# Kernel optimization log

Measured on AMD Instinct MI355X. Metric: run time of the kernel, lower is better.

The kernel has to match this reference:

```python
import jax, jax.numpy as jnp
import numpy as np

NUM_SCIENTISTS = 1_000_000
NUM_PAPERS = 100_000
EMB_DIM = 64
B = 262_144            # number of (scientist, paper) rating pairs
TOTAL_IMPLICIT = 5_242_880  # total flattened implicit-feedback paper ids (avg 20/row)
GLOBAL_MEAN = 3.82


def setup_inputs() -> dict:
    key = jax.random.key(0)
    ks = jax.random.split(key, 8)
    scientist_ids = jax.random.randint(ks[0], (B,), 0, NUM_SCIENTISTS, dtype=jnp.int32)
    paper_ids = jax.random.randint(ks[1], (B,), 0, NUM_PAPERS, dtype=jnp.int32)
    flat_papers = jax.random.randint(ks[2], (TOTAL_IMPLICIT,), 0, NUM_PAPERS, dtype=jnp.int32)
    # sorted segment ids: CSR-style ragged mapping implicit papers -> batch row
    segment_ids = jnp.sort(jax.random.randint(ks[3], (TOTAL_IMPLICIT,), 0, B, dtype=jnp.int32))
    scientist_factors = 0.1 * jax.random.normal(ks[4], (NUM_SCIENTISTS, EMB_DIM), dtype=jnp.float32)
    paper_factors = 0.1 * jax.random.normal(ks[5], (NUM_PAPERS, EMB_DIM), dtype=jnp.float32)
    implicit_factors = 0.1 * jax.random.normal(ks[6], (NUM_PAPERS, EMB_DIM), dtype=jnp.float32)
    scientist_bias = jnp.zeros((NUM_SCIENTISTS,), dtype=jnp.float32)
    paper_bias = jnp.zeros((NUM_PAPERS,), dtype=jnp.float32)
    return {
        "scientist_ids": scientist_ids,
        "paper_ids": paper_ids,
        "flat_papers": flat_papers,
        "segment_ids": segment_ids,
        "scientist_factors": scientist_factors,
        "paper_factors": paper_factors,
        "implicit_factors": implicit_factors,
        "scientist_bias": scientist_bias,
        "paper_bias": paper_bias,
    }


def reference(scientist_ids, paper_ids, flat_papers, segment_ids,
              scientist_factors, paper_factors, implicit_factors,
              scientist_bias, paper_bias):
    # explicit embedding gathers
    s_emb = scientist_factors[scientist_ids]          # [B, D]
    p_emb = paper_factors[paper_ids]                  # [B, D]
    s_b = scientist_bias[scientist_ids]               # [B]
    p_b = paper_bias[paper_ids]                       # [B]

    # ragged implicit-feedback gather + per-row sum (segment reduction)
    y_j = implicit_factors[flat_papers]               # [T, D]
    sum_yj = jax.ops.segment_sum(y_j, segment_ids, num_segments=B)       # [B, D]
    counts = jax.ops.segment_sum(jnp.ones_like(segment_ids, dtype=jnp.float32),
                                 segment_ids, num_segments=B)            # [B]
    # rows with empty history -> zero vector (matches the `if sp` branch)
    inv_sqrt = jnp.where(counts > 0, 1.0 / jnp.sqrt(jnp.maximum(counts, 1.0)), 0.0)
    y_u = sum_yj * inv_sqrt[:, None]                  # [B, D]

    interaction = jnp.sum((s_emb + y_u) * p_emb, axis=1)  # [B]
    return interaction + s_b + p_b + jnp.float32(GLOBAL_MEAN)
```

## Files before the change

### kernel.cpp

```cpp
#include <hip/hip_runtime.h>

#define EMB 64
#define CHUNK 256

#if defined(__has_builtin)
#if __has_builtin(__builtin_amdgcn_sdot4)
#define USE_SDOT 1
#endif
#endif
#ifndef USE_SDOT
#define USE_SDOT 0
#endif

__global__ __launch_bounds__(256) void prep_kernel(
    const int* __restrict__ seg, int* __restrict__ row_start, int T, int B,
    const float* __restrict__ src, uint* __restrict__ dst,
    float* __restrict__ scales, int nrows, int segBlocks) {
    if ((int)blockIdx.x < segBlocks) {
        const int t = (int)blockIdx.x * (int)blockDim.x + (int)threadIdx.x;
        if (t >= T) return;
        const int s  = seg[t];
        const int sp = (t == 0) ? -1 : seg[t - 1];
        for (int b = sp + 1; b <= s; ++b) row_start[b] = t;
        if (t == T - 1) {
            for (int b = s + 1; b <= B; ++b) row_start[b] = T;
        }
    } else {
        const int wave = (int)(((size_t)((int)blockIdx.x - segBlocks) * blockDim.x + threadIdx.x) >> 6);
        const int lane = (int)threadIdx.x & 63;
        const int g = lane >> 3, sub = lane & 7;
        const int r = wave * 8 + g;
        if (r >= nrows) return;

        const float* p = src + (size_t)r * EMB + (sub << 3);
        float e[8];
        #pragma unroll
        for (int k = 0; k < 8; ++k) e[k] = p[k];
        float mx = 0.f;
        #pragma unroll
        for (int k = 0; k < 8; ++k) mx = fmaxf(mx, fabsf(e[k]));
        mx = fmaxf(mx, __shfl_xor(mx, 1, 64));
        mx = fmaxf(mx, __shfl_xor(mx, 2, 64));
        mx = fmaxf(mx, __shfl_xor(mx, 4, 64));

        const float scale = mx * (1.0f / 7.0f);
        const float inv   = (mx > 0.f) ? (7.0f / mx) : 0.f;

        uint w = 0;
        #pragma unroll
        for (int k = 0; k < 8; ++k) {
            int q = (int)rintf(e[k] * inv);
            q = q < -7 ? -7 : (q > 7 ? 7 : q);
            w |= ((uint)(q + 8)) << (4 * k);
        }
        dst[(size_t)r * 8 + sub] = w;
        if (sub == 0) scales[r] = scale;
    }
}

__global__ __launch_bounds__(256) void svdpp_main_q4(
    const int*   __restrict__ scientist_ids,
    const int*   __restrict__ paper_ids,
    const int*   __restrict__ flat_papers,
    const int*   __restrict__ row_start,
    const float* __restrict__ scientist_factors,
    const float* __restrict__ paper_factors,
    const uint*  __restrict__ imp_q4,
    const float* __restrict__ imp_scale,
    const float* __restrict__ scientist_bias,
    const float* __restrict__ paper_bias,
    float*       __restrict__ out,
    int B) {
    const int wave = (int)((blockIdx.x * blockDim.x + threadIdx.x) >> 6);
    const int lane = threadIdx.x & 63;
    const int g    = lane >> 3;
    const int sub  = lane & 7;
    const int b0   = wave * 8;
    if (b0 >= B) return;
    const bool valid = (b0 + g) < B;
    const int b = valid ? (b0 + g) : (B - 1);
    const int w = (int)(threadIdx.x >> 6);

    __shared__ int lds_ids[4][CHUNK];

    const int sid   = __builtin_nontemporal_load(scientist_ids + b);
    const int pid   = __builtin_nontemporal_load(paper_ids + b);
    const int start = row_start[b];
    const int end   = row_start[b + 1];

    const int S = __shfl(start, 0, 64);
    const int E = __shfl(end, 63, 64);

    const float4* pf = reinterpret_cast<const float4*>(
        paper_factors + ((size_t)pid << 6)) + 2 * sub;
    const float4 pe0 = pf[0];
    const float4 pe1 = pf[1];

    const float* sf = scientist_factors + ((size_t)sid << 6) + (sub << 3);
    float se[8];
    #pragma unroll
    for (int k = 0; k < 8; ++k) se[k] = __builtin_nontemporal_load(sf + k);

    const float sb = __builtin_nontemporal_load(scientist_bias + sid);
    const float pb = __builtin_nontemporal_load(paper_bias + pid);

    const float base = se[0]*pe0.x + se[1]*pe0.y + se[2]*pe0.z + se[3]*pe0.w
                     + se[4]*pe1.x + se[5]*pe1.y + se[6]*pe1.z + se[7]*pe1.w;

#if USE_SDOT
    float pmax = fmaxf(fmaxf(fmaxf(fabsf(pe0.x), fabsf(pe0.y)),
                             fmaxf(fabsf(pe0.z), fabsf(pe0.w))),
                       fmaxf(fmaxf(fabsf(pe1.x), fabsf(pe1.y)),
                             fmaxf(fabsf(pe1.z), fabsf(pe1.w))));
    const float sp   = pmax * (1.0f / 127.0f);
    const float pinv = (pmax > 0.f) ? (127.0f / pmax) : 0.f;
    int qp[8];
    qp[0] = (int)rintf(pe0.x * pinv); qp[1] = (int)rintf(pe0.y * pinv);
    qp[2] = (int)rintf(pe0.z * pinv); qp[3] = (int)rintf(pe0.w * pinv);
    qp[4] = (int)rintf(pe1.x * pinv); qp[5] = (int)rintf(pe1.y * pinv);
    qp[6] = (int)rintf(pe1.z * pinv); qp[7] = (int)rintf(pe1.w * pinv);
    const int plo = (qp[0] & 0xff) | ((qp[2] & 0xff) << 8)
                  | ((qp[4] & 0xff) << 16) | ((qp[6] & 0xff) << 24);
    const int phi = (qp[1] & 0xff) | ((qp[3] & 0xff) << 8)
                  | ((qp[5] & 0xff) << 16) | ((qp[7] & 0xff) << 24);
    const int m8psum = -8 * (qp[0] + qp[1] + qp[2] + qp[3]
                           + qp[4] + qp[5] + qp[6] + qp[7]);
    const uint M = 0x0F0F0F0Fu;

    float A0 = 0.f, A1 = 0.f, A2 = 0.f, A3 = 0.f;
    for (int clo = S; clo < E; clo += CHUNK) {
        const int chi = (clo + CHUNK < E) ? (clo + CHUNK) : E;
        #pragma unroll
        for (int k = 0; k < CHUNK / 64; ++k) {
            const int idx = clo + lane + k * 64;
            if (idx < chi) lds_ids[w][lane + k * 64] = flat_papers[idx];
        }
        int ge = (start > clo) ? start : clo;
        const int gend = (end < chi) ? end : chi;
        for (; ge + 4 <= gend; ge += 4) {
            const int li = ge - clo;
            const int p0 = lds_ids[w][li];
            const int p1 = lds_ids[w][li + 1];
            const int p2 = lds_ids[w][li + 2];
            const int p3 = lds_ids[w][li + 3];
            const uint u0 = imp_q4[((size_t)p0 << 3) + sub];
            const uint u1 = imp_q4[((size_t)p1 << 3) + sub];
            const uint u2 = imp_q4[((size_t)p2 << 3) + sub];
            const uint u3 = imp_q4[((size_t)p3 << 3) + sub];
            const float s0 = imp_scale[p0];
            const float s1 = imp_scale[p1];
            const float s2 = imp_scale[p2];
            const float s3 = imp_scale[p3];
            const int d0 = __builtin_amdgcn_sdot4((int)(u0 & M), plo,
                           __builtin_amdgcn_sdot4((int)((u0 >> 4) & M), phi, m8psum, false), false);
            const int d1 = __builtin_amdgcn_sdot4((int)(u1 & M), plo,
                           __builtin_amdgcn_sdot4((int)((u1 >> 4) & M), phi, m8psum, false), false);
            const int d2 = __builtin_amdgcn_sdot4((int)(u2 & M), plo,
                           __builtin_amdgcn_sdot4((int)((u2 >> 4) & M), phi, m8psum, false), false);
            const int d3 = __builtin_amdgcn_sdot4((int)(u3 & M), plo,
                           __builtin_amdgcn_sdot4((int)((u3 >> 4) & M), phi, m8psum, false), false);
            A0 = fmaf(s0, (float)d0, A0);
            A1 = fmaf(s1, (float)d1, A1);
            A2 = fmaf(s2, (float)d2, A2);
            A3 = fmaf(s3, (float)d3, A3);
        }
        for (; ge < gend; ++ge) {
            const int p = lds_ids[w][ge - clo];
            const uint u = imp_q4[((size_t)p << 3) + sub];
            const float s = imp_scale[p];
            const int d = __builtin_amdgcn_sdot4((int)(u & M), plo,
                          __builtin_amdgcn_sdot4((int)((u >> 4) & M), phi, m8psum, false), false);
            A0 = fmaf(s, (float)d, A0);
        }
    }
    const float acc = sp * ((A0 + A1) + (A2 + A3));
#else
    const float pesum = pe0.x + pe0.y + pe0.z + pe0.w
                      + pe1.x + pe1.y + pe1.z + pe1.w;
    float A0 = 0.f, S0 = 0.f;
    for (int clo = S; clo < E; clo += CHUNK) {
        const int chi = (clo + CHUNK < E) ? (clo + CHUNK) : E;
        #pragma unroll
        for (int k = 0; k < CHUNK / 64; ++k) {
            const int idx = clo + lane + k * 64;
            if (idx < chi) lds_ids[w][lane + k * 64] = flat_papers[idx];
        }
        int ge = (start > clo) ? start : clo;
        const int gend = (end < chi) ? end : chi;
        for (; ge < gend; ++ge) {
            const int p = lds_ids[w][ge - clo];
            const uint u = imp_q4[((size_t)p << 3) + sub];
            const float s = imp_scale[p];
            const uint lo = u & 0x0F0F0F0Fu, hi = (u >> 4) & 0x0F0F0F0Fu;
            const float d = (float)(lo & 0xffu)*pe0.x + (float)(hi & 0xffu)*pe0.y
                          + (float)((lo >> 8) & 0xffu)*pe0.z + (float)((hi >> 8) & 0xffu)*pe0.w
                          + (float)((lo >> 16) & 0xffu)*pe1.x + (float)((hi >> 16) & 0xffu)*pe1.y
                          + (float)(lo >> 24)*pe1.z + (float)(hi >> 24)*pe1.w;
            A0 = fmaf(s, d, A0);  S0 += s;
        }
    }
    const float acc = A0 - 8.0f * S0 * pesum;
#endif

    const int n = end - start;
    const float scale = (n > 0) ? rsqrtf((float)n) : 0.0f;
    float v = base + scale * acc;

    v += __shfl_xor(v, 1, 64);
    v += __shfl_xor(v, 2, 64);
    v += __shfl_xor(v, 4, 64);

    if (sub == 0 && valid) {
        __builtin_nontemporal_store(v + sb + pb + 3.82f, out + (b0 + g));
    }
}

__global__ __launch_bounds__(256) void svdpp_main_f32(
    const int*   __restrict__ scientist_ids,
    const int*   __restrict__ paper_ids,
    const int*   __restrict__ flat_papers,
    const int*   __restrict__ row_start,
    const float* __restrict__ scientist_factors,
    const float* __restrict__ paper_factors,
    const float* __restrict__ implicit_factors,
    const float* __restrict__ scientist_bias,
    const float* __restrict__ paper_bias,
    float*       __restrict__ out,
    int B) {
    const int wave = (int)((blockIdx.x * blockDim.x + threadIdx.x) >> 6);
    const int lane = threadIdx.x & 63;
    if (wave >= B) return;
    const int b   = wave;
    const int g   = lane >> 4;
    const int sub = lane & 15;

    const int start = row_start[b];
    const int end   = row_start[b + 1];
    const int n     = end - start;

    float4 accA = make_float4(0.f,0.f,0.f,0.f);
    int i = start;
    for (; i < end; i += 4) {
        const int e = i + g;
        if (e < end) {
            const int p = flat_papers[e];
            const float4 r = *reinterpret_cast<const float4*>(
                implicit_factors + ((size_t)p << 6) + (sub << 2));
            accA.x += r.x; accA.y += r.y; accA.z += r.z; accA.w += r.w;
        }
    }

    const float scale = (n > 0) ? rsqrtf((float)n) : 0.0f;
    const int sid = scientist_ids[b];
    const int pid = paper_ids[b];
    const float4 se = *reinterpret_cast<const float4*>(
        scientist_factors + ((size_t)sid << 6) + (sub << 2));
    const float4 pe = *reinterpret_cast<const float4*>(
        paper_factors + ((size_t)pid << 6) + (sub << 2));

    const float basedot = se.x*pe.x + se.y*pe.y + se.z*pe.z + se.w*pe.w;
    const float tdot    = accA.x*pe.x + accA.y*pe.y + accA.z*pe.z + accA.w*pe.w;
    float v = scale * tdot + ((g == 0) ? basedot : 0.0f);

    #pragma unroll
    for (int off = 1; off < 64; off <<= 1) v += __shfl_xor(v, off, 64);

    if (lane == 0) {
        out[b] = v + scientist_bias[sid] + paper_bias[pid] + 3.82f;
    }
}

extern "C" void kernel_launch(void* const* d_in, const int* in_sizes, int n_in,
                              void* d_out, int out_size, void* d_ws, size_t ws_size,
                              hipStream_t stream) {
    const int* scientist_ids       = (const int*)d_in[0];
    const int* paper_ids           = (const int*)d_in[1];
    const int* flat_papers         = (const int*)d_in[2];
    const int* segment_ids         = (const int*)d_in[3];
    const float* scientist_factors = (const float*)d_in[4];
    const float* paper_factors     = (const float*)d_in[5];
    const float* implicit_factors  = (const float*)d_in[6];
    const float* scientist_bias    = (const float*)d_in[7];
    const float* paper_bias        = (const float*)d_in[8];
    float* out = (float*)d_out;

    const int B      = in_sizes[0];
    const int T      = in_sizes[2];
    const int IMP_N  = in_sizes[6];
    const int NROWS  = IMP_N / EMB;

    auto align64 = [](size_t x) { return (x + 63) & ~(size_t)63; };
    size_t off0 = 0;
    size_t off1 = align64(off0 + (size_t)(B + 1) * 4);
    size_t off2 = align64(off1 + (size_t)NROWS * 32);
    const size_t need = off2 + (size_t)NROWS * 4;

    int*   row_start  = (int*)((char*)d_ws + off0);
    uint*  imp_q4     = (uint*)((char*)d_ws + off1);
    float* imp_scale  = (float*)((char*)d_ws + off2);

    if (ws_size >= need) {
        {
            const int threads   = 256;
            const int segBlocks = (T + threads - 1) / threads;
            const int cvtBlocks = (NROWS + 31) / 32;
            prep_kernel<<<segBlocks + cvtBlocks, threads, 0, stream>>>(
                segment_ids, row_start, T, B,
                implicit_factors, imp_q4, imp_scale, NROWS, segBlocks);
        }
        {
            const int threads = 256;
            const int blocks  = (B + 31) / 32;
            svdpp_main_q4<<<blocks, threads, 0, stream>>>(
                scientist_ids, paper_ids, flat_papers, row_start,
                scientist_factors, paper_factors, imp_q4, imp_scale,
                scientist_bias, paper_bias, out, B);
        }
    } else {
        {
            const int threads = 256;
            const int blocks  = (T + threads - 1) / threads;
            prep_kernel<<<blocks, threads, 0, stream>>>(
                segment_ids, row_start, T, B,
                implicit_factors, (uint*)nullptr, (float*)nullptr, 0, blocks);
        }
        const int threads = 256;
        const int blocks  = (B + 3) / 4;
        svdpp_main_f32<<<blocks, threads, 0, stream>>>(
            scientist_ids, paper_ids, flat_papers, row_start,
            scientist_factors, paper_factors, implicit_factors,
            scientist_bias, paper_bias, out, B);
    }
}
```

Before: 105.0 us.

## Split each row's 8 lanes into two quads processing two implicit items in parallel

Each group of 8 lanes now splits into two halves of 4 lanes. Each lane loads a uint2 (16 dims) of the packed int4 implicit row, and the two halves handle alternating implicit items. This halves the serial gather iterations per row and widens each load to 8 bytes, at the cost of more registers for the paper vector and redundant scientist/paper loads in the second half. The base dot product and the tail handling are masked so only one half contributes where work is duplicated.

```diff
diff --git a/kernel.cpp b/kernel.cpp
--- a/kernel.cpp
+++ b/kernel.cpp
@@ -75,6 +75,8 @@
     const int lane = threadIdx.x & 63;
     const int g    = lane >> 3;
     const int sub  = lane & 7;
+    const int q    = sub & 3;
+    const int pairSel = sub >> 2;
     const int b0   = wave * 8;
     if (b0 >= B) return;
     const bool valid = (b0 + g) < B;
@@ -92,42 +94,60 @@
     const int E = __shfl(end, 63, 64);
 
     const float4* pf = reinterpret_cast<const float4*>(
-        paper_factors + ((size_t)pid << 6)) + 2 * sub;
-    const float4 pe0 = pf[0];
-    const float4 pe1 = pf[1];
-
-    const float* sf = scientist_factors + ((size_t)sid << 6) + (sub << 3);
-    float se[8];
-    #pragma unroll
-    for (int k = 0; k < 8; ++k) se[k] = __builtin_nontemporal_load(sf + k);
+        paper_factors + ((size_t)pid << 6)) + 4 * q;
+    const float4 pe0 = pf[0], pe1 = pf[1], pe2 = pf[2], pe3 = pf[3];
+
+    float base = 0.f;
+    {
+        const float* sf = scientist_factors + ((size_t)sid << 6) + (q << 4);
+        float se[16];
+        #pragma unroll
+        for (int k = 0; k < 16; ++k) se[k] = __builtin_nontemporal_load(sf + k);
+        const float bd =
+              se[0]*pe0.x + se[1]*pe0.y + se[2]*pe0.z + se[3]*pe0.w
+            + se[4]*pe1.x + se[5]*pe1.y + se[6]*pe1.z + se[7]*pe1.w
+            + se[8]*pe2.x + se[9]*pe2.y + se[10]*pe2.z + se[11]*pe2.w
+            + se[12]*pe3.x + se[13]*pe3.y + se[14]*pe3.z + se[15]*pe3.w;
+        base = (pairSel == 0) ? bd : 0.f;
+    }
 
     const float sb = __builtin_nontemporal_load(scientist_bias + sid);
     const float pb = __builtin_nontemporal_load(paper_bias + pid);
 
-    const float base = se[0]*pe0.x + se[1]*pe0.y + se[2]*pe0.z + se[3]*pe0.w
-                     + se[4]*pe1.x + se[5]*pe1.y + se[6]*pe1.z + se[7]*pe1.w;
-
 #if USE_SDOT
-    float pmax = fmaxf(fmaxf(fmaxf(fabsf(pe0.x), fabsf(pe0.y)),
-                             fmaxf(fabsf(pe0.z), fabsf(pe0.w))),
-                       fmaxf(fmaxf(fabsf(pe1.x), fabsf(pe1.y)),
-                             fmaxf(fabsf(pe1.z), fabsf(pe1.w))));
+    float pmax = 0.f;
+    {
+        pmax = fmaxf(pmax, fmaxf(fmaxf(fabsf(pe0.x), fabsf(pe0.y)), fmaxf(fabsf(pe0.z), fabsf(pe0.w))));
+        pmax = fmaxf(pmax, fmaxf(fmaxf(fabsf(pe1.x), fabsf(pe1.y)), fmaxf(fabsf(pe1.z), fabsf(pe1.w))));
+        pmax = fmaxf(pmax, fmaxf(fmaxf(fabsf(pe2.x), fabsf(pe2.y)), fmaxf(fabsf(pe2.z), fabsf(pe2.w))));
+        pmax = fmaxf(pmax, fmaxf(fmaxf(fabsf(pe3.x), fabsf(pe3.y)), fmaxf(fabsf(pe3.z), fabsf(pe3.w))));
+    }
     const float sp   = pmax * (1.0f / 127.0f);
     const float pinv = (pmax > 0.f) ? (127.0f / pmax) : 0.f;
-    int qp[8];
-    qp[0] = (int)rintf(pe0.x * pinv); qp[1] = (int)rintf(pe0.y * pinv);
-    qp[2] = (int)rintf(pe0.z * pinv); qp[3] = (int)rintf(pe0.w * pinv);
-    qp[4] = (int)rintf(pe1.x * pinv); qp[5] = (int)rintf(pe1.y * pinv);
-    qp[6] = (int)rintf(pe1.z * pinv); qp[7] = (int)rintf(pe1.w * pinv);
-    const int plo = (qp[0] & 0xff) | ((qp[2] & 0xff) << 8)
-                  | ((qp[4] & 0xff) << 16) | ((qp[6] & 0xff) << 24);
-    const int phi = (qp[1] & 0xff) | ((qp[3] & 0xff) << 8)
-                  | ((qp[5] & 0xff) << 16) | ((qp[7] & 0xff) << 24);
-    const int m8psum = -8 * (qp[0] + qp[1] + qp[2] + qp[3]
-                           + qp[4] + qp[5] + qp[6] + qp[7]);
+    int plo[2], phi[2];
+    int psum = 0;
+    {
+        const int q0 = (int)rintf(pe0.x * pinv), q1 = (int)rintf(pe0.y * pinv);
+        const int q2 = (int)rintf(pe0.z * pinv), q3 = (int)rintf(pe0.w * pinv);
+        const int q4v = (int)rintf(pe1.x * pinv), q5 = (int)rintf(pe1.y * pinv);
+        const int q6 = (int)rintf(pe1.z * pinv), q7 = (int)rintf(pe1.w * pinv);
+        plo[0] = (q0 & 0xff) | ((q2 & 0xff) << 8) | ((q4v & 0xff) << 16) | ((q6 & 0xff) << 24);
+        phi[0] = (q1 & 0xff) | ((q3 & 0xff) << 8) | ((q5 & 0xff) << 16) | ((q7 & 0xff) << 24);
+        psum += (q0 + q1) + (q2 + q3) + (q4v + q5) + (q6 + q7);
+    }
+    {
+        const int q0 = (int)rintf(pe2.x * pinv), q1 = (int)rintf(pe2.y * pinv);
+        const int q2 = (int)rintf(pe2.z * pinv), q3 = (int)rintf(pe2.w * pinv);
+        const int q4v = (int)rintf(pe3.x * pinv), q5 = (int)rintf(pe3.y * pinv);
+        const int q6 = (int)rintf(pe3.z * pinv), q7 = (int)rintf(pe3.w * pinv);
+        plo[1] = (q0 & 0xff) | ((q2 & 0xff) << 8) | ((q4v & 0xff) << 16) | ((q6 & 0xff) << 24);
+        phi[1] = (q1 & 0xff) | ((q3 & 0xff) << 8) | ((q5 & 0xff) << 16) | ((q7 & 0xff) << 24);
+        psum += (q0 + q1) + (q2 + q3) + (q4v + q5) + (q6 + q7);
+    }
+    const int m8psum = -8 * psum;
     const uint M = 0x0F0F0F0Fu;
 
-    float A0 = 0.f, A1 = 0.f, A2 = 0.f, A3 = 0.f;
+    float A0 = 0.f, A1 = 0.f;
     for (int clo = S; clo < E; clo += CHUNK) {
         const int chi = (clo + CHUNK < E) ? (clo + CHUNK) : E;
         #pragma unroll
@@ -139,44 +159,54 @@
         const int gend = (end < chi) ? end : chi;
         for (; ge + 4 <= gend; ge += 4) {
             const int li = ge - clo;
-            const int p0 = lds_ids[w][li];
-            const int p1 = lds_ids[w][li + 1];
-            const int p2 = lds_ids[w][li + 2];
-            const int p3 = lds_ids[w][li + 3];
-            const uint u0 = imp_q4[((size_t)p0 << 3) + sub];
-            const uint u1 = imp_q4[((size_t)p1 << 3) + sub];
-            const uint u2 = imp_q4[((size_t)p2 << 3) + sub];
-            const uint u3 = imp_q4[((size_t)p3 << 3) + sub];
-            const float s0 = imp_scale[p0];
-            const float s1 = imp_scale[p1];
-            const float s2 = imp_scale[p2];
-            const float s3 = imp_scale[p3];
-            const int d0 = __builtin_amdgcn_sdot4((int)(u0 & M), plo,
-                           __builtin_amdgcn_sdot4((int)((u0 >> 4) & M), phi, m8psum, false), false);
-            const int d1 = __builtin_amdgcn_sdot4((int)(u1 & M), plo,
-                           __builtin_amdgcn_sdot4((int)((u1 >> 4) & M), phi, m8psum, false), false);
-            const int d2 = __builtin_amdgcn_sdot4((int)(u2 & M), plo,
-                           __builtin_amdgcn_sdot4((int)((u2 >> 4) & M), phi, m8psum, false), false);
-            const int d3 = __builtin_amdgcn_sdot4((int)(u3 & M), plo,
-                           __builtin_amdgcn_sdot4((int)((u3 >> 4) & M), phi, m8psum, false), false);
-            A0 = fmaf(s0, (float)d0, A0);
-            A1 = fmaf(s1, (float)d1, A1);
-            A2 = fmaf(s2, (float)d2, A2);
-            A3 = fmaf(s3, (float)d3, A3);
-        }
-        for (; ge < gend; ++ge) {
+            const int pA = lds_ids[w][li + pairSel];
+            const int pB = lds_ids[w][li + 2 + pairSel];
+            const uint2 uA = reinterpret_cast<const uint2*>(imp_q4 + ((size_t)pA << 3))[q];
+            const uint2 uB = reinterpret_cast<const uint2*>(imp_q4 + ((size_t)pB << 3))[q];
+            const float sA = imp_scale[pA];
+            const float sB = imp_scale[pB];
+            int dA = m8psum;
+            dA = __builtin_amdgcn_sdot4((int)(uA.x & M), plo[0], dA, false);
+            dA = __builtin_amdgcn_sdot4((int)((uA.x >> 4) & M), phi[0], dA, false);
+            dA = __builtin_amdgcn_sdot4((int)(uA.y & M), plo[1], dA, false);
+            dA = __builtin_amdgcn_sdot4((int)((uA.y >> 4) & M), phi[1], dA, false);
+            int dB = m8psum;
+            dB = __builtin_amdgcn_sdot4((int)(uB.x & M), plo[0], dB, false);
+            dB = __builtin_amdgcn_sdot4((int)((uB.x >> 4) & M), phi[0], dB, false);
+            dB = __builtin_amdgcn_sdot4((int)(uB.y & M), plo[1], dB, false);
+            dB = __builtin_amdgcn_sdot4((int)((uB.y >> 4) & M), phi[1], dB, false);
+            A0 = fmaf(sA, (float)dA, A0);
+            A1 = fmaf(sB, (float)dB, A1);
+        }
+        if (ge + 2 <= gend) {
+            const int li = ge - clo;
+            const int p = lds_ids[w][li + pairSel];
+            const uint2 u = reinterpret_cast<const uint2*>(imp_q4 + ((size_t)p << 3))[q];
+            const float s = imp_scale[p];
+            int d = m8psum;
+            d = __builtin_amdgcn_sdot4((int)(u.x & M), plo[0], d, false);
+            d = __builtin_amdgcn_sdot4((int)((u.x >> 4) & M), phi[0], d, false);
+            d = __builtin_amdgcn_sdot4((int)(u.y & M), plo[1], d, false);
+            d = __builtin_amdgcn_sdot4((int)((u.y >> 4) & M), phi[1], d, false);
+            A0 = fmaf(s, (float)d, A0);
+            ge += 2;
+        }
+        if (ge < gend) {
             const int p = lds_ids[w][ge - clo];
-            const uint u = imp_q4[((size_t)p << 3) + sub];
+            const uint2 u = reinterpret_cast<const uint2*>(imp_q4 + ((size_t)p << 3))[q];
             const float s = imp_scale[p];
-            const int d = __builtin_amdgcn_sdot4((int)(u & M), plo,
-                          __builtin_amdgcn_sdot4((int)((u >> 4) & M), phi, m8psum, false), false);
-            A0 = fmaf(s, (float)d, A0);
-        }
-    }
-    const float acc = sp * ((A0 + A1) + (A2 + A3));
+            int d = m8psum;
+            d = __builtin_amdgcn_sdot4((int)(u.x & M), plo[0], d, false);
+            d = __builtin_amdgcn_sdot4((int)((u.x >> 4) & M), phi[0], d, false);
+            d = __builtin_amdgcn_sdot4((int)(u.y & M), plo[1], d, false);
+            d = __builtin_amdgcn_sdot4((int)((u.y >> 4) & M), phi[1], d, false);
+            if (pairSel == 0) A0 = fmaf(s, (float)d, A0);
+        }
+    }
+    const float acc = sp * (A0 + A1);
 #else
-    const float pesum = pe0.x + pe0.y + pe0.z + pe0.w
-                      + pe1.x + pe1.y + pe1.z + pe1.w;
+    float pesum = pe0.x+pe0.y+pe0.z+pe0.w + pe1.x+pe1.y+pe1.z+pe1.w
+                + pe2.x+pe2.y+pe2.z+pe2.w + pe3.x+pe3.y+pe3.z+pe3.w;
     float A0 = 0.f, S0 = 0.f;
     for (int clo = S; clo < E; clo += CHUNK) {
         const int chi = (clo + CHUNK < E) ? (clo + CHUNK) : E;
@@ -189,22 +219,32 @@
         const int gend = (end < chi) ? end : chi;
         for (; ge < gend; ++ge) {
             const int p = lds_ids[w][ge - clo];
-            const uint u = imp_q4[((size_t)p << 3) + sub];
+            const uint2 u = reinterpret_cast<const uint2*>(imp_q4 + ((size_t)p << 3))[q];
             const float s = imp_scale[p];
-            const uint lo = u & 0x0F0F0F0Fu, hi = (u >> 4) & 0x0F0F0F0Fu;
-            const float d = (float)(lo & 0xffu)*pe0.x + (float)(hi & 0xffu)*pe0.y
-                          + (float)((lo >> 8) & 0xffu)*pe0.z + (float)((hi >> 8) & 0xffu)*pe0.w
-                          + (float)((lo >> 16) & 0xffu)*pe1.x + (float)((hi >> 16) & 0xffu)*pe1.y
-                          + (float)(lo >> 24)*pe1.z + (float)(hi >> 24)*pe1.w;
-            A0 = fmaf(s, d, A0);  S0 += s;
+            float d = 0.f;
+            {
+                const uint lo = u.x & 0x0F0F0F0Fu, hi = (u.x >> 4) & 0x0F0F0F0Fu;
+                d += (float)(lo & 0xffu)*pe0.x + (float)(hi & 0xffu)*pe0.y
+                   + (float)((lo >> 8) & 0xffu)*pe0.z + (float)((hi >> 8) & 0xffu)*pe0.w
+                   + (float)((lo >> 16) & 0xffu)*pe1.x + (float)((hi >> 16) & 0xffu)*pe1.y
+                   + (float)(lo >> 24)*pe1.z + (float)(hi >> 24)*pe1.w;
+            }
+            {
+                const uint lo = u.y & 0x0F0F0F0Fu, hi = (u.y >> 4) & 0x0F0F0F0Fu;
+                d += (float)(lo & 0xffu)*pe2.x + (float)(hi & 0xffu)*pe2.y
+                   + (float)((lo >> 8) & 0xffu)*pe2.z + (float)((hi >> 8) & 0xffu)*pe2.w
+                   + (float)((lo >> 16) & 0xffu)*pe3.x + (float)((hi >> 16) & 0xffu)*pe3.y
+                   + (float)(lo >> 24)*pe3.z + (float)(hi >> 24)*pe3.w;
+            }
+            if (pairSel == 0) { A0 = fmaf(s, d, A0); S0 += s; }
         }
     }
     const float acc = A0 - 8.0f * S0 * pesum;
 #endif
 
     const int n = end - start;
-    const float scale = (n > 0) ? rsqrtf((float)n) : 0.0f;
-    float v = base + scale * acc;
+    const float scl = (n > 0) ? rsqrtf((float)n) : 0.0f;
+    float v = base + scl * acc;
 
     v += __shfl_xor(v, 1, 64);
     v += __shfl_xor(v, 2, 64);
```

New measurement: 115.5 us. 1.1x slower.

## Stage implicit ids per block in shared LDS chunk with block-wide sync

Applied to the files above, without the earlier changes.

Each 256-thread block now handles 32 consecutive rows and cooperatively loads the block's whole contiguous range of flat_papers into one shared 512-entry LDS buffer, replacing the per-wave 256-entry buffers. Every wave reads ids from the shared buffer, and __syncthreads brackets each chunk. This cuts the number of chunk iterations and makes the id loads wider and coalesced across the block. In exchange, waves are now coupled by barriers, so imbalance in row lengths between waves can stall the whole block.

```diff
diff --git a/kernel.cpp b/kernel.cpp
--- a/kernel.cpp
+++ b/kernel.cpp
@@ -1,7 +1,7 @@
 #include <hip/hip_runtime.h>
 
 #define EMB 64
-#define CHUNK 256
+#define CHUNK 512
 
 #if defined(__has_builtin)
 #if __has_builtin(__builtin_amdgcn_sdot4)
@@ -71,25 +71,26 @@
     const float* __restrict__ paper_bias,
     float*       __restrict__ out,
     int B) {
-    const int wave = (int)((blockIdx.x * blockDim.x + threadIdx.x) >> 6);
-    const int lane = threadIdx.x & 63;
+    const int tid  = (int)threadIdx.x;
+    const int lane = tid & 63;
+    const int wv   = tid >> 6;
     const int g    = lane >> 3;
     const int sub  = lane & 7;
-    const int b0   = wave * 8;
-    if (b0 >= B) return;
-    const bool valid = (b0 + g) < B;
-    const int b = valid ? (b0 + g) : (B - 1);
-    const int w = (int)(threadIdx.x >> 6);
-
-    __shared__ int lds_ids[4][CHUNK];
+    const int bb0  = (int)blockIdx.x * 32;
+    const int myrow = bb0 + wv * 8 + g;
+    const bool valid = myrow < B;
+    const int b = valid ? myrow : (B - 1);
+
+    __shared__ int lds_ids[CHUNK];
+
+    int ehi = bb0 + 32; if (ehi > B) ehi = B;
+    const int S_blk = row_start[bb0];
+    const int E_blk = row_start[ehi];
 
     const int sid   = __builtin_nontemporal_load(scientist_ids + b);
     const int pid   = __builtin_nontemporal_load(paper_ids + b);
     const int start = row_start[b];
     const int end   = row_start[b + 1];
-
-    const int S = __shfl(start, 0, 64);
-    const int E = __shfl(end, 63, 64);
 
     const float4* pf = reinterpret_cast<const float4*>(
         paper_factors + ((size_t)pid << 6)) + 2 * sub;
@@ -128,21 +129,20 @@
     const uint M = 0x0F0F0F0Fu;
 
     float A0 = 0.f, A1 = 0.f, A2 = 0.f, A3 = 0.f;
-    for (int clo = S; clo < E; clo += CHUNK) {
-        const int chi = (clo + CHUNK < E) ? (clo + CHUNK) : E;
-        #pragma unroll
-        for (int k = 0; k < CHUNK / 64; ++k) {
-            const int idx = clo + lane + k * 64;
-            if (idx < chi) lds_ids[w][lane + k * 64] = flat_papers[idx];
-        }
+    for (int clo = S_blk; clo < E_blk; clo += CHUNK) {
+        const int chi = (clo + CHUNK < E_blk) ? (clo + CHUNK) : E_blk;
+        for (int k = tid; k < chi - clo; k += 256) {
+            lds_ids[k] = flat_papers[clo + k];
+        }
+        __syncthreads();
         int ge = (start > clo) ? start : clo;
         const int gend = (end < chi) ? end : chi;
         for (; ge + 4 <= gend; ge += 4) {
             const int li = ge - clo;
-            const int p0 = lds_ids[w][li];
-            const int p1 = lds_ids[w][li + 1];
-            const int p2 = lds_ids[w][li + 2];
-            const int p3 = lds_ids[w][li + 3];
+            const int p0 = lds_ids[li];
+            const int p1 = lds_ids[li + 1];
+            const int p2 = lds_ids[li + 2];
+            const int p3 = lds_ids[li + 3];
             const uint u0 = imp_q4[((size_t)p0 << 3) + sub];
             const uint u1 = imp_q4[((size_t)p1 << 3) + sub];
             const uint u2 = imp_q4[((size_t)p2 << 3) + sub];
@@ -165,30 +165,30 @@
             A3 = fmaf(s3, (float)d3, A3);
         }
         for (; ge < gend; ++ge) {
-            const int p = lds_ids[w][ge - clo];
+            const int p = lds_ids[ge - clo];
             const uint u = imp_q4[((size_t)p << 3) + sub];
             const float s = imp_scale[p];
             const int d = __builtin_amdgcn_sdot4((int)(u & M), plo,
                           __builtin_amdgcn_sdot4((int)((u >> 4) & M), phi, m8psum, false), false);
             A0 = fmaf(s, (float)d, A0);
         }
+        __syncthreads();
     }
     const float acc = sp * ((A0 + A1) + (A2 + A3));
 #else
     const float pesum = pe0.x + pe0.y + pe0.z + pe0.w
                       + pe1.x + pe1.y + pe1.z + pe1.w;
     float A0 = 0.f, S0 = 0.f;
-    for (int clo = S; clo < E; clo += CHUNK) {
-        const int chi = (clo + CHUNK < E) ? (clo + CHUNK) : E;
-        #pragma unroll
-        for (int k = 0; k < CHUNK / 64; ++k) {
-            const int idx = clo + lane + k * 64;
-            if (idx < chi) lds_ids[w][lane + k * 64] = flat_papers[idx];
-        }
+    for (int clo = S_blk; clo < E_blk; clo += CHUNK) {
+        const int chi = (clo + CHUNK < E_blk) ? (clo + CHUNK) : E_blk;
+        for (int k = tid; k < chi - clo; k += 256) {
+            lds_ids[k] = flat_papers[clo + k];
+        }
+        __syncthreads();
         int ge = (start > clo) ? start : clo;
         const int gend = (end < chi) ? end : chi;
         for (; ge < gend; ++ge) {
-            const int p = lds_ids[w][ge - clo];
+            const int p = lds_ids[ge - clo];
             const uint u = imp_q4[((size_t)p << 3) + sub];
             const float s = imp_scale[p];
             const uint lo = u & 0x0F0F0F0Fu, hi = (u >> 4) & 0x0F0F0F0Fu;
@@ -198,6 +198,7 @@
                           + (float)(lo >> 24)*pe1.z + (float)(hi >> 24)*pe1.w;
             A0 = fmaf(s, d, A0);  S0 += s;
         }
+        __syncthreads();
     }
     const float acc = A0 - 8.0f * S0 * pesum;
 #endif
@@ -211,7 +212,7 @@
     v += __shfl_xor(v, 4, 64);
 
     if (sub == 0 && valid) {
-        __builtin_nontemporal_store(v + sb + pb + 3.82f, out + (b0 + g));
+        __builtin_nontemporal_store(v + sb + pb + 3.82f, out + myrow);
     }
 }
 
```

Measured after the change: 115.4 us. 9.9% more time.
